# Kernel optimization log

Measured on AMD Instinct MI355X. Metric: run time of the kernel, lower is better.

The kernel has to match this reference:

```python
import jax, jax.numpy as jnp
import numpy as np

N = 100000      # nodes
E = 1600000     # edges (avg degree 16)
D = 64          # in_channels == conv widths == lin width
G = 64          # graphs in batch
OUT = 10        # out_channels


def setup_inputs() -> dict:
    key = jax.random.key(0)
    ks = jax.random.split(key, 20)
    s = 0.1
    inp = {
        "x": jax.random.normal(ks[0], (N, D), jnp.float32),
        "edge_index": jax.random.randint(ks[1], (2, E), 0, N, dtype=jnp.int64),
        "batch": jnp.sort(jax.random.randint(ks[2], (N,), 0, G, dtype=jnp.int64)),
    }
    k = 3
    for i in range(3):  # 3 SAGEConv layers: lin_l (Wl, bl) on aggregated, lin_r (Wr, no bias) on root
        inp[f"c{i}_Wl"] = jax.random.normal(ks[k], (D, D), jnp.float32) * s; k += 1
        inp[f"c{i}_bl"] = jnp.zeros((D,), jnp.float32)
        inp[f"c{i}_Wr"] = jax.random.normal(ks[k], (D, D), jnp.float32) * s; k += 1
    inp["l0_W"] = jax.random.normal(ks[k], (D, D), jnp.float32) * s; k += 1
    inp["l0_b"] = jnp.zeros((D,), jnp.float32)
    inp["out_W"] = jax.random.normal(ks[k], (D, OUT), jnp.float32) * s; k += 1
    inp["out_b"] = jnp.zeros((OUT,), jnp.float32)
    return inp


def reference(x, edge_index, batch,
              c0_Wl, c0_bl, c0_Wr,
              c1_Wl, c1_bl, c1_Wr,
              c2_Wl, c2_bl, c2_Wr,
              l0_W, l0_b, out_W, out_b):
    src, dst = edge_index[0], edge_index[1]
    # in-degree of each target node (mean conv aggregation), computed once
    deg = jax.ops.segment_sum(jnp.ones((E,), x.dtype), dst, num_segments=N)
    inv_deg = (1.0 / jnp.maximum(deg, 1.0))[:, None]

    def sage(h, Wl, bl, Wr):
        # gather source features, mean-aggregate at targets, then lin_l(agg) + lin_r(h)
        agg = jax.ops.segment_sum(h[src], dst, num_segments=N) * inv_deg
        return agg @ Wl + bl + h @ Wr

    h = jax.nn.relu(sage(x, c0_Wl, c0_bl, c0_Wr))
    h = jax.nn.relu(sage(h, c1_Wl, c1_bl, c1_Wr))
    h = jax.nn.relu(sage(h, c2_Wl, c2_bl, c2_Wr))

    # global mean pool over graphs
    cnt = jax.ops.segment_sum(jnp.ones((N,), h.dtype), batch, num_segments=G)
    g = jax.ops.segment_sum(h, batch, num_segments=G) / jnp.maximum(cnt, 1.0)[:, None]

    g = jax.nn.relu(g @ l0_W + l0_b)
    return g @ out_W + out_b  # [G, OUT]
```

## Files before the change

### kernel.cpp

```cpp
#include <hip/hip_runtime.h>
#include <hip/hip_fp16.h>

#define WPB 8
#define PADK 136
#define BSH 8
#define BNODES 256
#define SC_BLOCKS 256
#define HIST_BLOCKS 256
#define HSTRIDE 512

typedef _Float16 half8 __attribute__((ext_vector_type(8)));
typedef _Float16 half4v __attribute__((ext_vector_type(4)));
typedef float floatx4 __attribute__((ext_vector_type(4)));

__global__ __launch_bounds__(256) void gnn_pre(const int* __restrict__ dst,
                                               int* __restrict__ bkt_cnt, int nbkt, int E,
                                               const int* __restrict__ batch,
                                               float* __restrict__ gcnt, int N,
                                               const float4* __restrict__ xin,
                                               ushort4* __restrict__ x16o, int n4,
                                               __half* __restrict__ x16,
                                               __half* __restrict__ hA,
                                               __half* __restrict__ hB,
                                               int* __restrict__ hist_all) {
    int tid = threadIdx.x;
    if (blockIdx.x < HIST_BLOCKS) {
        __shared__ int h[512];
        __shared__ int gb[64];
        for (int i = tid; i < nbkt; i += 256) h[i] = 0;
        if (tid < 64) gb[tid] = 0;
        __syncthreads();
        const int stride = HIST_BLOCKS * 256;
        if ((E & 3) == 0) {
            const int4* dst4 = (const int4*)dst;
            int E4 = E >> 2;
            for (int e = blockIdx.x * 256 + tid; e < E4; e += stride) {
                int4 d = dst4[e];
                atomicAdd(&h[d.x >> BSH], 1);
                atomicAdd(&h[d.y >> BSH], 1);
                atomicAdd(&h[d.z >> BSH], 1);
                atomicAdd(&h[d.w >> BSH], 1);
            }
        } else {
            for (int e = blockIdx.x * 256 + tid; e < E; e += stride)
                atomicAdd(&h[dst[e] >> BSH], 1);
        }
        for (int i = blockIdx.x * 256 + tid; i < N; i += stride)
            atomicAdd(&gb[batch[i]], 1);
        __syncthreads();
        for (int i = tid; i < nbkt; i += 256) {
            int v = h[i];
            hist_all[blockIdx.x * HSTRIDE + i] = v;
            if (v) atomicAdd(&bkt_cnt[i], v);
        }
        if (tid < 64) {
            int v = gb[tid];
            if (v) atomicAdd(&gcnt[tid], (float)v);
        }
        if (blockIdx.x == 0 && tid < 64) {
            x16[(size_t)N * 64 + tid] = __ushort_as_half((unsigned short)0);
            hA[(size_t)N * 64 + tid] = __ushort_as_half((unsigned short)0);
            hB[(size_t)N * 64 + tid] = __ushort_as_half((unsigned short)0);
        }
    } else {
        int i = (blockIdx.x - HIST_BLOCKS) * 256 + tid;
        if (i < n4) {
            float4 f = xin[i];
            ushort4 o;
            o.x = __half_as_ushort(__float2half(f.x));
            o.y = __half_as_ushort(__float2half(f.y));
            o.z = __half_as_ushort(__float2half(f.z));
            o.w = __half_as_ushort(__float2half(f.w));
            x16o[i] = o;
        }
    }
}

__global__ void gnn_bkt_scan(const int* __restrict__ bkt_cnt, int* __restrict__ bkt_base,
                             int* __restrict__ row_ptr, int nbkt, int N) {
    int lane = threadIdx.x;
    int carry = 0;
    for (int base = 0; base < nbkt; base += 64) {
        int idx = base + lane;
        int v = (idx < nbkt) ? bkt_cnt[idx] : 0;
        int x = v;
#pragma unroll
        for (int off = 1; off < 64; off <<= 1) {
            int y = __shfl_up(x, off);
            if (lane >= off) x += y;
        }
        if (idx < nbkt) bkt_base[idx] = carry + (x - v);
        carry += __shfl(x, 63);
    }
    if (lane == 0) {
        bkt_base[nbkt] = carry;
        row_ptr[N] = carry;
    }
}

__global__ __launch_bounds__(256) void gnn_scan2(const int* __restrict__ hist_all,
                                                 const int* __restrict__ bkt_base,
                                                 int* __restrict__ blk_base_all, int nbkt) {
    int b = blockIdx.x;
    int t = threadIdx.x, lane = t & 63, wv = t >> 6;
    __shared__ int wsum[4];
    int v = hist_all[t * HSTRIDE + b];
    int x = v;
#pragma unroll
    for (int off = 1; off < 64; off <<= 1) {
        int y = __shfl_up(x, off);
        if (lane >= off) x += y;
    }
    if (lane == 63) wsum[wv] = x;
    __syncthreads();
    int wexcl = 0;
    for (int w = 0; w < wv; w++) wexcl += wsum[w];
    blk_base_all[t * HSTRIDE + b] = bkt_base[b] + wexcl + (x - v);
}

__global__ __launch_bounds__(256) void gnn_bkt_scatter(const int* __restrict__ src,
                                                       const int* __restrict__ dst,
                                                       const int* __restrict__ blk_base_all,
                                                       unsigned int* __restrict__ pairs,
                                                       int E, int nbkt) {
    __shared__ int cur[512];
    int tid = threadIdx.x;
    for (int i = tid; i < nbkt; i += 256) cur[i] = blk_base_all[blockIdx.x * HSTRIDE + i];
    __syncthreads();
    const int stride = SC_BLOCKS * 256;
    if ((E & 3) == 0) {
        const int4* dst4 = (const int4*)dst;
        const int4* src4 = (const int4*)src;
        int E4 = E >> 2;
        for (int e = blockIdx.x * 256 + tid; e < E4; e += stride) {
            int4 d = dst4[e];
            int4 s = src4[e];
            int p0 = atomicAdd(&cur[d.x >> BSH], 1);
            pairs[p0] = (unsigned int)s.x | ((unsigned int)(d.x & (BNODES - 1)) << 24);
            int p1 = atomicAdd(&cur[d.y >> BSH], 1);
            pairs[p1] = (unsigned int)s.y | ((unsigned int)(d.y & (BNODES - 1)) << 24);
            int p2 = atomicAdd(&cur[d.z >> BSH], 1);
            pairs[p2] = (unsigned int)s.z | ((unsigned int)(d.z & (BNODES - 1)) << 24);
            int p3 = atomicAdd(&cur[d.w >> BSH], 1);
            pairs[p3] = (unsigned int)s.w | ((unsigned int)(d.w & (BNODES - 1)) << 24);
        }
    } else {
        for (int e = blockIdx.x * 256 + tid; e < E; e += stride) {
            int d = dst[e];
            int b = d >> BSH;
            int p = atomicAdd(&cur[b], 1);
            pairs[p] = (unsigned int)src[e] | ((unsigned int)(d & (BNODES - 1)) << 24);
        }
    }
}

__global__ __launch_bounds__(256) void gnn_bkt_csr(const unsigned int* __restrict__ pairs,
                                                   const int* __restrict__ bkt_base,
                                                   int* __restrict__ row_ptr,
                                                   float* __restrict__ inv_deg,
                                                   int* __restrict__ csr_src, int N) {
    __shared__ int hist[BNODES];
    __shared__ int excl[BNODES];
    __shared__ int cur[BNODES];
    int b = blockIdx.x;
    int base = bkt_base[b];
    int cnt = bkt_base[b + 1] - base;
    int nd0 = b << BSH;
    int tid = threadIdx.x;
    hist[tid] = 0;
    __syncthreads();
    {
        int a0 = (4 - (base & 3)) & 3;
        a0 = min(a0, cnt);
        for (int i = tid; i < a0; i += 256) atomicAdd(&hist[pairs[base + i] >> 24], 1);
        int vcnt = (cnt - a0) >> 2;
        const uint4* p4 = (const uint4*)(pairs + base + a0);
        for (int i = tid; i < vcnt; i += 256) {
            uint4 u = p4[i];
            atomicAdd(&hist[u.x >> 24], 1);
            atomicAdd(&hist[u.y >> 24], 1);
            atomicAdd(&hist[u.z >> 24], 1);
            atomicAdd(&hist[u.w >> 24], 1);
        }
        for (int i = a0 + (vcnt << 2) + tid; i < cnt; i += 256)
            atomicAdd(&hist[pairs[base + i] >> 24], 1);
    }
    __syncthreads();
    if (tid < 64) {
        int carry = 0;
#pragma unroll
        for (int c = 0; c < BNODES; c += 64) {
            int v = hist[c + tid];
            int x = v;
#pragma unroll
            for (int off = 1; off < 64; off <<= 1) {
                int y = __shfl_up(x, off);
                if (tid >= off) x += y;
            }
            excl[c + tid] = carry + (x - v);
            carry += __shfl(x, 63);
        }
    }
    __syncthreads();
    {
        int node = nd0 + tid;
        if (node < N) {
            row_ptr[node] = base + excl[tid];
            int d = hist[tid];
            inv_deg[node] = 1.0f / (float)(d > 1 ? d : 1);
        }
        cur[tid] = excl[tid];
    }
    __syncthreads();
    {
        int a0 = (4 - (base & 3)) & 3;
        a0 = min(a0, cnt);
        for (int i = tid; i < a0; i += 256) {
            unsigned int u = pairs[base + i];
            int pos = atomicAdd(&cur[u >> 24], 1);
            csr_src[base + pos] = (int)(u & 0xFFFFFFu);
        }
        int vcnt = (cnt - a0) >> 2;
        const uint4* p4 = (const uint4*)(pairs + base + a0);
        for (int i = tid; i < vcnt; i += 256) {
            uint4 u = p4[i];
            int pos0 = atomicAdd(&cur[u.x >> 24], 1);
            csr_src[base + pos0] = (int)(u.x & 0xFFFFFFu);
            int pos1 = atomicAdd(&cur[u.y >> 24], 1);
            csr_src[base + pos1] = (int)(u.y & 0xFFFFFFu);
            int pos2 = atomicAdd(&cur[u.z >> 24], 1);
            csr_src[base + pos2] = (int)(u.z & 0xFFFFFFu);
            int pos3 = atomicAdd(&cur[u.w >> 24], 1);
            csr_src[base + pos3] = (int)(u.w & 0xFFFFFFu);
        }
        for (int i = a0 + (vcnt << 2) + tid; i < cnt; i += 256) {
            unsigned int u = pairs[base + i];
            int pos = atomicAdd(&cur[u >> 24], 1);
            csr_src[base + pos] = (int)(u & 0xFFFFFFu);
        }
    }
}

#define LOAD4(eReg, c0, vArr)                                  \
    _Pragma("unroll") for (int c_ = 0; c_ < 4; c_++) {         \
        int sj_ = __shfl(eReg, (c0) + c_ * 4 + quad);          \
        vArr[c_] = hin4v[(size_t)sj_ * 16 + m16];              \
    }
#define ACC4(vArr, accum)                                      \
    _Pragma("unroll") for (int c_ = 0; c_ < 4; c_++) {         \
        accum.x += (float)vArr[c_][0];                         \
        accum.y += (float)vArr[c_][1];                         \
        accum.z += (float)vArr[c_][2];                         \
        accum.w += (float)vArr[c_][3];                         \
    }

__global__ __launch_bounds__(512, 4) void gnn_sage(const __half* __restrict__ hin,
                                                   __half* __restrict__ hout,
                                                   const int* __restrict__ row_ptr,
                                                   const int* __restrict__ csr_src,
                                                   const float* __restrict__ inv_deg,
                                                   const float* __restrict__ Wl,
                                                   const float* __restrict__ bl,
                                                   const float* __restrict__ Wr, int n) {
    __shared__ _Float16 w_lds[64 * PADK];
    __shared__ _Float16 in_lds[WPB][16 * PADK];
    int tid = threadIdx.x, lane = tid & 63, wv = tid >> 6;
    for (int i = tid; i < 64 * 64; i += 512) {
        int k = i >> 6, nn = i & 63;
        w_lds[nn * PADK + k] = (_Float16)Wl[i];
        w_lds[nn * PADK + 64 + k] = (_Float16)Wr[i];
    }
    __syncthreads();
    int ngroups = (n + 15) >> 4;
    int g = blockIdx.x * WPB + wv;
    if (g >= ngroups) return;
    int m16 = lane & 15, quad = lane >> 4;
    int hf = lane >> 5, col = lane & 31;
    float bias[4];
#pragma unroll
    for (int nt = 0; nt < 4; nt++) bias[nt] = bl[nt * 16 + m16];
    _Float16* my_in = in_lds[wv];
    const unsigned* hin32 = (const unsigned*)hin;
    const half4v* hin4v = (const half4v*)hin;
    int nd0 = g << 4;
    int nclamp = n - 1 - nd0;
    int idx = nd0 + lane;
    int rr = (lane <= 16) ? row_ptr[min(idx, n)] : 0;
    float ig = (lane < 16) ? inv_deg[min(idx, n - 1)] : 0.0f;

#pragma unroll
    for (int jp = 0; jp < 8; jp++) {
        int j2 = jp << 1;
        int nd = nd0 + min(j2 + hf, nclamp);
        unsigned u = hin32[(size_t)nd * 32 + col];
        ((unsigned*)(my_in + (j2 + hf) * PADK + 64))[col] = u;
    }

    int ef[16];
#pragma unroll
    for (int j = 0; j < 16; j++) {
        int jj = min(j, nclamp);
        int s0 = __shfl(rr, jj), s1 = __shfl(rr, jj + 1);
        int cb = min(64, s1 - s0);
        ef[j] = (lane < cb) ? csr_src[s0 + lane] : n;
    }

#pragma unroll
    for (int jp = 0; jp < 8; jp++) {
        int j2 = jp << 1;
        int jjA = min(j2, nclamp), jjB = min(j2 + 1, nclamp);
        int s0A = __shfl(rr, jjA), s1A = __shfl(rr, jjA + 1);
        int s0B = __shfl(rr, jjB), s1B = __shfl(rr, jjB + 1);
        float idgA = __shfl(ig, jjA), idgB = __shfl(ig, jjB);
        int cbA = min(64, s1A - s0A), cbB = min(64, s1B - s0B);
        floatx4 accA = {0.f, 0.f, 0.f, 0.f};
        floatx4 accB = {0.f, 0.f, 0.f, 0.f};
        {
            half4v vA[4], vB[4];
            LOAD4(ef[j2], 0, vA);
            LOAD4(ef[j2 + 1], 0, vB);
            ACC4(vA, accA);
            ACC4(vB, accB);
        }
        if (cbA > 16) {
            half4v v0[4];
            LOAD4(ef[j2], 16, v0);
            ACC4(v0, accA);
            if (cbA > 32) { half4v v1[4]; LOAD4(ef[j2], 32, v1); ACC4(v1, accA); }
            if (cbA > 48) { half4v v2[4]; LOAD4(ef[j2], 48, v2); ACC4(v2, accA); }
        }
        if (cbB > 16) {
            half4v v0[4];
            LOAD4(ef[j2 + 1], 16, v0);
            ACC4(v0, accB);
            if (cbB > 32) { half4v v1[4]; LOAD4(ef[j2 + 1], 32, v1); ACC4(v1, accB); }
            if (cbB > 48) { half4v v2[4]; LOAD4(ef[j2 + 1], 48, v2); ACC4(v2, accB); }
        }
        for (int base_ = s0A + 64; base_ < s1A; base_ += 64) {
            int cb = min(64, s1A - base_);
            int ei = (lane < cb) ? csr_src[base_ + lane] : n;
            for (int i0 = 0; i0 < cb; i0 += 16) {
                half4v vt[4];
                LOAD4(ei, i0, vt);
                ACC4(vt, accA);
            }
        }
        for (int base_ = s0B + 64; base_ < s1B; base_ += 64) {
            int cb = min(64, s1B - base_);
            int ei = (lane < cb) ? csr_src[base_ + lane] : n;
            for (int i0 = 0; i0 < cb; i0 += 16) {
                half4v vt[4];
                LOAD4(ei, i0, vt);
                ACC4(vt, accB);
            }
        }
        accA.x += __shfl_xor(accA.x, 16); accA.y += __shfl_xor(accA.y, 16);
        accA.z += __shfl_xor(accA.z, 16); accA.w += __shfl_xor(accA.w, 16);
        accA.x += __shfl_xor(accA.x, 32); accA.y += __shfl_xor(accA.y, 32);
        accA.z += __shfl_xor(accA.z, 32); accA.w += __shfl_xor(accA.w, 32);
        accB.x += __shfl_xor(accB.x, 16); accB.y += __shfl_xor(accB.y, 16);
        accB.z += __shfl_xor(accB.z, 16); accB.w += __shfl_xor(accB.w, 16);
        accB.x += __shfl_xor(accB.x, 32); accB.y += __shfl_xor(accB.y, 32);
        accB.z += __shfl_xor(accB.z, 32); accB.w += __shfl_xor(accB.w, 32);
        if (quad == 0) {
            half4v hw;
            hw[0] = (_Float16)(accA.x * idgA);
            hw[1] = (_Float16)(accA.y * idgA);
            hw[2] = (_Float16)(accA.z * idgA);
            hw[3] = (_Float16)(accA.w * idgA);
            *(half4v*)(my_in + j2 * PADK + m16 * 4) = hw;
        } else if (quad == 1) {
            half4v hw;
            hw[0] = (_Float16)(accB.x * idgB);
            hw[1] = (_Float16)(accB.y * idgB);
            hw[2] = (_Float16)(accB.z * idgB);
            hw[3] = (_Float16)(accB.w * idgB);
            *(half4v*)(my_in + (j2 + 1) * PADK + m16 * 4) = hw;
        }
    }
    half8 afrag[4];
    const _Float16* abase = my_in + m16 * PADK + quad * 8;
#pragma unroll
    for (int ks = 0; ks < 4; ks++) afrag[ks] = *(const half8*)(abase + ks * 32);
    floatx4 accv[4];
#pragma unroll
    for (int nt = 0; nt < 4; nt++) {
        accv[nt].x = 0.f; accv[nt].y = 0.f; accv[nt].z = 0.f; accv[nt].w = 0.f;
    }
#pragma unroll
    for (int nt = 0; nt < 4; nt++) {
        const _Float16* bbase = w_lds + (nt * 16 + m16) * PADK + quad * 8;
#pragma unroll
        for (int ks = 0; ks < 4; ks++) {
            half8 bfrag = *(const half8*)(bbase + ks * 32);
            accv[nt] = __builtin_amdgcn_mfma_f32_16x16x32_f16(afrag[ks], bfrag, accv[nt], 0, 0, 0);
        }
    }
#pragma unroll
    for (int nt = 0; nt < 4; nt++) {
#pragma unroll
        for (int r = 0; r < 4; r++) {
            int node = nd0 + quad * 4 + r;
            if (node < n) {
                float v = fmaxf(accv[nt][r] + bias[nt], 0.0f);
                hout[(size_t)node * 64 + nt * 16 + m16] = __float2half(v);
            }
        }
    }
}

__global__ __launch_bounds__(512, 4) void gnn_sage_pool(const __half* __restrict__ hin,
                                                        const int* __restrict__ row_ptr,
                                                        const int* __restrict__ csr_src,
                                                        const float* __restrict__ inv_deg,
                                                        const float* __restrict__ Wl,
                                                        const float* __restrict__ bl,
                                                        const float* __restrict__ Wr,
                                                        const int* __restrict__ batch,
                                                        float* __restrict__ gsum, int n) {
    __shared__ _Float16 w_lds[64 * PADK];
    __shared__ _Float16 in_lds[WPB][16 * PADK];
    int tid = threadIdx.x, lane = tid & 63, wv = tid >> 6;
    for (int i = tid; i < 64 * 64; i += 512) {
        int k = i >> 6, nn = i & 63;
        w_lds[nn * PADK + k] = (_Float16)Wl[i];
        w_lds[nn * PADK + 64 + k] = (_Float16)Wr[i];
    }
    __syncthreads();
    int ngroups = (n + 15) >> 4;
    int g = blockIdx.x * WPB + wv;
    if (g >= ngroups) return;
    int m16 = lane & 15, quad = lane >> 4;
    int hf = lane >> 5, col = lane & 31;
    float bias[4];
#pragma unroll
    for (int nt = 0; nt < 4; nt++) bias[nt] = bl[nt * 16 + m16];
    _Float16* my_in = in_lds[wv];
    const unsigned* hin32 = (const unsigned*)hin;
    const half4v* hin4v = (const half4v*)hin;
    int nd0 = g << 4;
    int nclamp = n - 1 - nd0;
    int idx = nd0 + lane;
    int rr = (lane <= 16) ? row_ptr[min(idx, n)] : 0;
    float ig = (lane < 16) ? inv_deg[min(idx, n - 1)] : 0.0f;

#pragma unroll
    for (int jp = 0; jp < 8; jp++) {
        int j2 = jp << 1;
        int nd = nd0 + min(j2 + hf, nclamp);
        unsigned u = hin32[(size_t)nd * 32 + col];
        ((unsigned*)(my_in + (j2 + hf) * PADK + 64))[col] = u;
    }

    int ef[16];
#pragma unroll
    for (int j = 0; j < 16; j++) {
        int jj = min(j, nclamp);
        int s0 = __shfl(rr, jj), s1 = __shfl(rr, jj + 1);
        int cb = min(64, s1 - s0);
        ef[j] = (lane < cb) ? csr_src[s0 + lane] : n;
    }

#pragma unroll
    for (int jp = 0; jp < 8; jp++) {
        int j2 = jp << 1;
        int jjA = min(j2, nclamp), jjB = min(j2 + 1, nclamp);
        int s0A = __shfl(rr, jjA), s1A = __shfl(rr, jjA + 1);
        int s0B = __shfl(rr, jjB), s1B = __shfl(rr, jjB + 1);
        float idgA = __shfl(ig, jjA), idgB = __shfl(ig, jjB);
        int cbA = min(64, s1A - s0A), cbB = min(64, s1B - s0B);
        floatx4 accA = {0.f, 0.f, 0.f, 0.f};
        floatx4 accB = {0.f, 0.f, 0.f, 0.f};
        {
            half4v vA[4], vB[4];
            LOAD4(ef[j2], 0, vA);
            LOAD4(ef[j2 + 1], 0, vB);
            ACC4(vA, accA);
            ACC4(vB, accB);
        }
        if (cbA > 16) {
            half4v v0[4];
            LOAD4(ef[j2], 16, v0);
            ACC4(v0, accA);
            if (cbA > 32) { half4v v1[4]; LOAD4(ef[j2], 32, v1); ACC4(v1, accA); }
            if (cbA > 48) { half4v v2[4]; LOAD4(ef[j2], 48, v2); ACC4(v2, accA); }
        }
        if (cbB > 16) {
            half4v v0[4];
            LOAD4(ef[j2 + 1], 16, v0);
            ACC4(v0, accB);
            if (cbB > 32) { half4v v1[4]; LOAD4(ef[j2 + 1], 32, v1); ACC4(v1, accB); }
            if (cbB > 48) { half4v v2[4]; LOAD4(ef[j2 + 1], 48, v2); ACC4(v2, accB); }
        }
        for (int base_ = s0A + 64; base_ < s1A; base_ += 64) {
            int cb = min(64, s1A - base_);
            int ei = (lane < cb) ? csr_src[base_ + lane] : n;
            for (int i0 = 0; i0 < cb; i0 += 16) {
                half4v vt[4];
                LOAD4(ei, i0, vt);
                ACC4(vt, accA);
            }
        }
        for (int base_ = s0B + 64; base_ < s1B; base_ += 64) {
            int cb = min(64, s1B - base_);
            int ei = (lane < cb) ? csr_src[base_ + lane] : n;
            for (int i0 = 0; i0 < cb; i0 += 16) {
                half4v vt[4];
                LOAD4(ei, i0, vt);
                ACC4(vt, accB);
            }
        }
        accA.x += __shfl_xor(accA.x, 16); accA.y += __shfl_xor(accA.y, 16);
        accA.z += __shfl_xor(accA.z, 16); accA.w += __shfl_xor(accA.w, 16);
        accA.x += __shfl_xor(accA.x, 32); accA.y += __shfl_xor(accA.y, 32);
        accA.z += __shfl_xor(accA.z, 32); accA.w += __shfl_xor(accA.w, 32);
        accB.x += __shfl_xor(accB.x, 16); accB.y += __shfl_xor(accB.y, 16);
        accB.z += __shfl_xor(accB.z, 16); accB.w += __shfl_xor(accB.w, 16);
        accB.x += __shfl_xor(accB.x, 32); accB.y += __shfl_xor(accB.y, 32);
        accB.z += __shfl_xor(accB.z, 32); accB.w += __shfl_xor(accB.w, 32);
        if (quad == 0) {
            half4v hw;
            hw[0] = (_Float16)(accA.x * idgA);
            hw[1] = (_Float16)(accA.y * idgA);
            hw[2] = (_Float16)(accA.z * idgA);
            hw[3] = (_Float16)(accA.w * idgA);
            *(half4v*)(my_in + j2 * PADK + m16 * 4) = hw;
        } else if (quad == 1) {
            half4v hw;
            hw[0] = (_Float16)(accB.x * idgB);
            hw[1] = (_Float16)(accB.y * idgB);
            hw[2] = (_Float16)(accB.z * idgB);
            hw[3] = (_Float16)(accB.w * idgB);
            *(half4v*)(my_in + (j2 + 1) * PADK + m16 * 4) = hw;
        }
    }
    half8 afrag[4];
    const _Float16* abase = my_in + m16 * PADK + quad * 8;
#pragma unroll
    for (int ks = 0; ks < 4; ks++) afrag[ks] = *(const half8*)(abase + ks * 32);
    floatx4 accv[4];
#pragma unroll
    for (int nt = 0; nt < 4; nt++) {
        accv[nt].x = 0.f; accv[nt].y = 0.f; accv[nt].z = 0.f; accv[nt].w = 0.f;
    }
#pragma unroll
    for (int nt = 0; nt < 4; nt++) {
        const _Float16* bbase = w_lds + (nt * 16 + m16) * PADK + quad * 8;
#pragma unroll
        for (int ks = 0; ks < 4; ks++) {
            half8 bfrag = *(const half8*)(bbase + ks * 32);
            accv[nt] = __builtin_amdgcn_mfma_f32_16x16x32_f16(afrag[ks], bfrag, accv[nt], 0, 0, 0);
        }
    }
    int bFirst = batch[nd0];
    int bLast = batch[min(nd0 + 15, n - 1)];
    if (bFirst == bLast && nd0 + 15 < n) {
#pragma unroll
        for (int nt = 0; nt < 4; nt++) {
            float s = fmaxf(accv[nt][0] + bias[nt], 0.0f) + fmaxf(accv[nt][1] + bias[nt], 0.0f) +
                      fmaxf(accv[nt][2] + bias[nt], 0.0f) + fmaxf(accv[nt][3] + bias[nt], 0.0f);
            s += __shfl_xor(s, 16);
            s += __shfl_xor(s, 32);
            if (quad == 0) atomicAdd(&gsum[bFirst * 64 + nt * 16 + m16], s);
        }
    } else {
#pragma unroll
        for (int nt = 0; nt < 4; nt++) {
#pragma unroll
            for (int r = 0; r < 4; r++) {
                int node = nd0 + quad * 4 + r;
                if (node < n) {
                    int bg = batch[node];
                    float v = fmaxf(accv[nt][r] + bias[nt], 0.0f);
                    atomicAdd(&gsum[bg * 64 + nt * 16 + m16], v);
                }
            }
        }
    }
}

__global__ __launch_bounds__(1024) void gnn_head(const float* __restrict__ gsum,
                                                 const float* __restrict__ gcnt,
                                                 const float* __restrict__ l0W,
                                                 const float* __restrict__ l0b,
                                                 const float* __restrict__ outW,
                                                 const float* __restrict__ outb,
                                                 float* __restrict__ out, int G, int OUT) {
    __shared__ float gm[64 * 64];
    __shared__ float t2[64 * 64];
    int tid = threadIdx.x;
    for (int i = tid; i < G * 64; i += 1024) {
        int r = i >> 6;
        gm[i] = gsum[i] / fmaxf(gcnt[r], 1.0f);
    }
    __syncthreads();
    for (int i = tid; i < G * 64; i += 1024) {
        int r = i >> 6, c = i & 63;
        float s = l0b[c];
#pragma unroll 8
        for (int k = 0; k < 64; k++) s += gm[(r << 6) + k] * l0W[(k << 6) + c];
        t2[i] = fmaxf(s, 0.0f);
    }
    __syncthreads();
    for (int i = tid; i < G * OUT; i += 1024) {
        int r = i / OUT, c = i - r * OUT;
        float s = outb[c];
#pragma unroll 8
        for (int k = 0; k < 64; k++) s += t2[(r << 6) + k] * outW[k * OUT + c];
        out[i] = s;
    }
}

extern "C" void kernel_launch(void* const* d_in, const int* in_sizes, int n_in,
                              void* d_out, int out_size, void* d_ws, size_t ws_size,
                              hipStream_t stream) {
    const float* x = (const float*)d_in[0];
    const int* ei = (const int*)d_in[1];
    const int* batch = (const int*)d_in[2];
    const float* Wl[3] = {(const float*)d_in[3], (const float*)d_in[6], (const float*)d_in[9]};
    const float* bl[3] = {(const float*)d_in[4], (const float*)d_in[7], (const float*)d_in[10]};
    const float* Wr[3] = {(const float*)d_in[5], (const float*)d_in[8], (const float*)d_in[11]};
    const float* l0W = (const float*)d_in[12];
    const float* l0b = (const float*)d_in[13];
    const float* outW = (const float*)d_in[14];
    const float* outb = (const float*)d_in[15];

    int N = in_sizes[2];
    int E = in_sizes[1] / 2;
    int OUT = 10;
    int G = out_size / OUT;
    const int* src = ei;
    const int* dst = ei + E;
    int NBKT = (N + BNODES - 1) >> BSH;

    char* ws = (char*)d_ws;
    size_t off = 0;
    auto alloc = [&](size_t b) -> char* {
        char* p = ws + off;
        off = (off + b + 255) & ~(size_t)255;
        return p;
    };
    int* row_ptr = (int*)alloc((size_t)(N + 1) * 4);
    int* csr_src = (int*)alloc((size_t)E * 4);
    float* inv_deg = (float*)alloc((size_t)N * 4);
    size_t zoff = off;
    int* bkt_cnt = (int*)alloc((size_t)NBKT * 4);
    float* gcnt = (float*)alloc((size_t)G * 4);
    float* gsum = (float*)alloc((size_t)G * 64 * 4);
    size_t zlen = off - zoff;
    int* bkt_base = (int*)alloc((size_t)(NBKT + 1) * 4);
    int* hist_all = (int*)alloc((size_t)HIST_BLOCKS * HSTRIDE * 4);
    int* blk_base_all = (int*)alloc((size_t)HIST_BLOCKS * HSTRIDE * 4);
    unsigned int* pairs = (unsigned int*)alloc((size_t)E * 4);
    __half* x16 = (__half*)alloc((size_t)(N + 1) * 64 * 2);
    __half* hA = (__half*)alloc((size_t)(N + 1) * 64 * 2);
    __half* hB = (__half*)alloc((size_t)(N + 1) * 64 * 2);

    hipMemsetAsync(ws + zoff, 0, zlen, stream);

    int n4 = N * 64 / 4;
    int pre_blocks = HIST_BLOCKS + (n4 + 255) / 256;
    gnn_pre<<<pre_blocks, 256, 0, stream>>>(dst, bkt_cnt, NBKT, E, batch, gcnt, N,
                                            (const float4*)x, (ushort4*)x16, n4,
                                            x16, hA, hB, hist_all);
    gnn_bkt_scan<<<1, 64, 0, stream>>>(bkt_cnt, bkt_base, row_ptr, NBKT, N);
    gnn_scan2<<<NBKT, 256, 0, stream>>>(hist_all, bkt_base, blk_base_all, NBKT);
    gnn_bkt_scatter<<<SC_BLOCKS, 256, 0, stream>>>(src, dst, blk_base_all, pairs, E, NBKT);
    gnn_bkt_csr<<<NBKT, 256, 0, stream>>>(pairs, bkt_base, row_ptr, inv_deg, csr_src, N);

    int ngroups = (N + 15) >> 4;
    int sage_blocks = (ngroups + WPB - 1) / WPB;
    gnn_sage<<<sage_blocks, 512, 0, stream>>>(x16, hA, row_ptr, csr_src, inv_deg,
                                              Wl[0], bl[0], Wr[0], N);
    gnn_sage<<<sage_blocks, 512, 0, stream>>>(hA, hB, row_ptr, csr_src, inv_deg,
                                              Wl[1], bl[1], Wr[1], N);
    gnn_sage_pool<<<sage_blocks, 512, 0, stream>>>(hB, row_ptr, csr_src, inv_deg,
                                                   Wl[2], bl[2], Wr[2], batch, gsum, N);

    gnn_head<<<1, 1024, 0, stream>>>(gsum, gcnt, l0W, l0b, outW, outb, (float*)d_out, G, OUT);
}
```

Before: 293.5 us.

## Fold bucket scan into scan2 and fuse MLP head into pool kernel

Removes two kernel launches. The single-block bucket prefix scan is dropped: each scan2 block now computes its own bucket base by reducing all preceding bucket counts, and the last block also writes the total. The separate one-block head kernel is folded into the final SAGE pooling kernel through a last-block-done atomic counter, and that last block runs the two small dense layers in reused shared memory. In exchange, scan2 blocks do redundant reduction work, and the head runs with 512 threads instead of 1024.

Result: slower. 304.5 us (+3.7%).

```diff
diff --git a/kernel.cpp b/kernel.cpp
--- a/kernel.cpp
+++ b/kernel.cpp
@@ -76,34 +76,21 @@
     }
 }
 
-__global__ void gnn_bkt_scan(const int* __restrict__ bkt_cnt, int* __restrict__ bkt_base,
-                             int* __restrict__ row_ptr, int nbkt, int N) {
-    int lane = threadIdx.x;
-    int carry = 0;
-    for (int base = 0; base < nbkt; base += 64) {
-        int idx = base + lane;
-        int v = (idx < nbkt) ? bkt_cnt[idx] : 0;
-        int x = v;
-#pragma unroll
-        for (int off = 1; off < 64; off <<= 1) {
-            int y = __shfl_up(x, off);
-            if (lane >= off) x += y;
-        }
-        if (idx < nbkt) bkt_base[idx] = carry + (x - v);
-        carry += __shfl(x, 63);
-    }
-    if (lane == 0) {
-        bkt_base[nbkt] = carry;
-        row_ptr[N] = carry;
-    }
-}
-
 __global__ __launch_bounds__(256) void gnn_scan2(const int* __restrict__ hist_all,
-                                                 const int* __restrict__ bkt_base,
-                                                 int* __restrict__ blk_base_all, int nbkt) {
+                                                 const int* __restrict__ bkt_cnt,
+                                                 int* __restrict__ bkt_base,
+                                                 int* __restrict__ row_ptr,
+                                                 int* __restrict__ blk_base_all,
+                                                 int nbkt, int N) {
     int b = blockIdx.x;
     int t = threadIdx.x, lane = t & 63, wv = t >> 6;
     __shared__ int wsum[4];
+    __shared__ int red[4];
+    int part = 0;
+    for (int i = t; i < b; i += 256) part += bkt_cnt[i];
+#pragma unroll
+    for (int off = 1; off < 64; off <<= 1) part += __shfl_xor(part, off);
+    if (lane == 0) red[wv] = part;
     int v = hist_all[t * HSTRIDE + b];
     int x = v;
 #pragma unroll
@@ -113,9 +100,18 @@
     }
     if (lane == 63) wsum[wv] = x;
     __syncthreads();
+    int base = red[0] + red[1] + red[2] + red[3];
     int wexcl = 0;
     for (int w = 0; w < wv; w++) wexcl += wsum[w];
-    blk_base_all[t * HSTRIDE + b] = bkt_base[b] + wexcl + (x - v);
+    blk_base_all[t * HSTRIDE + b] = base + wexcl + (x - v);
+    if (t == 0) {
+        bkt_base[b] = base;
+        if (b == nbkt - 1) {
+            int tot = base + bkt_cnt[b];
+            bkt_base[nbkt] = tot;
+            row_ptr[N] = tot;
+        }
+    }
 }
 
 __global__ __launch_bounds__(256) void gnn_bkt_scatter(const int* __restrict__ src,
@@ -417,9 +413,18 @@
                                                         const float* __restrict__ bl,
                                                         const float* __restrict__ Wr,
                                                         const int* __restrict__ batch,
-                                                        float* __restrict__ gsum, int n) {
+                                                        float* __restrict__ gsum,
+                                                        const float* __restrict__ gcnt,
+                                                        const float* __restrict__ l0W,
+                                                        const float* __restrict__ l0b,
+                                                        const float* __restrict__ outW,
+                                                        const float* __restrict__ outb,
+                                                        float* __restrict__ out,
+                                                        unsigned int* __restrict__ done,
+                                                        int G, int OUT, int n) {
     __shared__ _Float16 w_lds[64 * PADK];
     __shared__ _Float16 in_lds[WPB][16 * PADK];
+    __shared__ int lastsh;
     int tid = threadIdx.x, lane = tid & 63, wv = tid >> 6;
     for (int i = tid; i < 64 * 64; i += 512) {
         int k = i >> 6, nn = i & 63;
@@ -429,185 +434,186 @@
     __syncthreads();
     int ngroups = (n + 15) >> 4;
     int g = blockIdx.x * WPB + wv;
-    if (g >= ngroups) return;
     int m16 = lane & 15, quad = lane >> 4;
     int hf = lane >> 5, col = lane & 31;
-    float bias[4];
-#pragma unroll
-    for (int nt = 0; nt < 4; nt++) bias[nt] = bl[nt * 16 + m16];
-    _Float16* my_in = in_lds[wv];
     const unsigned* hin32 = (const unsigned*)hin;
     const half4v* hin4v = (const half4v*)hin;
-    int nd0 = g << 4;
-    int nclamp = n - 1 - nd0;
-    int idx = nd0 + lane;
-    int rr = (lane <= 16) ? row_ptr[min(idx, n)] : 0;
-    float ig = (lane < 16) ? inv_deg[min(idx, n - 1)] : 0.0f;
-
-#pragma unroll
-    for (int jp = 0; jp < 8; jp++) {
-        int j2 = jp << 1;
-        int nd = nd0 + min(j2 + hf, nclamp);
-        unsigned u = hin32[(size_t)nd * 32 + col];
-        ((unsigned*)(my_in + (j2 + hf) * PADK + 64))[col] = u;
-    }
-
-    int ef[16];
-#pragma unroll
-    for (int j = 0; j < 16; j++) {
-        int jj = min(j, nclamp);
-        int s0 = __shfl(rr, jj), s1 = __shfl(rr, jj + 1);
-        int cb = min(64, s1 - s0);
-        ef[j] = (lane < cb) ? csr_src[s0 + lane] : n;
-    }
-
-#pragma unroll
-    for (int jp = 0; jp < 8; jp++) {
-        int j2 = jp << 1;
-        int jjA = min(j2, nclamp), jjB = min(j2 + 1, nclamp);
-        int s0A = __shfl(rr, jjA), s1A = __shfl(rr, jjA + 1);
-        int s0B = __shfl(rr, jjB), s1B = __shfl(rr, jjB + 1);
-        float idgA = __shfl(ig, jjA), idgB = __shfl(ig, jjB);
-        int cbA = min(64, s1A - s0A), cbB = min(64, s1B - s0B);
-        floatx4 accA = {0.f, 0.f, 0.f, 0.f};
-        floatx4 accB = {0.f, 0.f, 0.f, 0.f};
-        {
-            half4v vA[4], vB[4];
-            LOAD4(ef[j2], 0, vA);
-            LOAD4(ef[j2 + 1], 0, vB);
-            ACC4(vA, accA);
-            ACC4(vB, accB);
-        }
-        if (cbA > 16) {
-            half4v v0[4];
-            LOAD4(ef[j2], 16, v0);
-            ACC4(v0, accA);
-            if (cbA > 32) { half4v v1[4]; LOAD4(ef[j2], 32, v1); ACC4(v1, accA); }
-            if (cbA > 48) { half4v v2[4]; LOAD4(ef[j2], 48, v2); ACC4(v2, accA); }
-        }
-        if (cbB > 16) {
-            half4v v0[4];
-            LOAD4(ef[j2 + 1], 16, v0);
-            ACC4(v0, accB);
-            if (cbB > 32) { half4v v1[4]; LOAD4(ef[j2 + 1], 32, v1); ACC4(v1, accB); }
-            if (cbB > 48) { half4v v2[4]; LOAD4(ef[j2 + 1], 48, v2); ACC4(v2, accB); }
-        }
-        for (int base_ = s0A + 64; base_ < s1A; base_ += 64) {
-            int cb = min(64, s1A - base_);
-            int ei = (lane < cb) ? csr_src[base_ + lane] : n;
-            for (int i0 = 0; i0 < cb; i0 += 16) {
-                half4v vt[4];
-                LOAD4(ei, i0, vt);
-                ACC4(vt, accA);
-            }
-        }
-        for (int base_ = s0B + 64; base_ < s1B; base_ += 64) {
-            int cb = min(64, s1B - base_);
-            int ei = (lane < cb) ? csr_src[base_ + lane] : n;
-            for (int i0 = 0; i0 < cb; i0 += 16) {
-                half4v vt[4];
-                LOAD4(ei, i0, vt);
-                ACC4(vt, accB);
-            }
-        }
-        accA.x += __shfl_xor(accA.x, 16); accA.y += __shfl_xor(accA.y, 16);
-        accA.z += __shfl_xor(accA.z, 16); accA.w += __shfl_xor(accA.w, 16);
-        accA.x += __shfl_xor(accA.x, 32); accA.y += __shfl_xor(accA.y, 32);
-        accA.z += __shfl_xor(accA.z, 32); accA.w += __shfl_xor(accA.w, 32);
-        accB.x += __shfl_xor(accB.x, 16); accB.y += __shfl_xor(accB.y, 16);
-        accB.z += __shfl_xor(accB.z, 16); accB.w += __shfl_xor(accB.w, 16);
-        accB.x += __shfl_xor(accB.x, 32); accB.y += __shfl_xor(accB.y, 32);
-        accB.z += __shfl_xor(accB.z, 32); accB.w += __shfl_xor(accB.w, 32);
-        if (quad == 0) {
-            half4v hw;
-            hw[0] = (_Float16)(accA.x * idgA);
-            hw[1] = (_Float16)(accA.y * idgA);
-            hw[2] = (_Float16)(accA.z * idgA);
-            hw[3] = (_Float16)(accA.w * idgA);
-            *(half4v*)(my_in + j2 * PADK + m16 * 4) = hw;
-        } else if (quad == 1) {
-            half4v hw;
-            hw[0] = (_Float16)(accB.x * idgB);
-            hw[1] = (_Float16)(accB.y * idgB);
-            hw[2] = (_Float16)(accB.z * idgB);
-            hw[3] = (_Float16)(accB.w * idgB);
-            *(half4v*)(my_in + (j2 + 1) * PADK + m16 * 4) = hw;
-        }
-    }
-    half8 afrag[4];
-    const _Float16* abase = my_in + m16 * PADK + quad * 8;
-#pragma unroll
-    for (int ks = 0; ks < 4; ks++) afrag[ks] = *(const half8*)(abase + ks * 32);
-    floatx4 accv[4];
-#pragma unroll
-    for (int nt = 0; nt < 4; nt++) {
-        accv[nt].x = 0.f; accv[nt].y = 0.f; accv[nt].z = 0.f; accv[nt].w = 0.f;
-    }
-#pragma unroll
-    for (int nt = 0; nt < 4; nt++) {
-        const _Float16* bbase = w_lds + (nt * 16 + m16) * PADK + quad * 8;
-#pragma unroll
-        for (int ks = 0; ks < 4; ks++) {
-            half8 bfrag = *(const half8*)(bbase + ks * 32);
-            accv[nt] = __builtin_amdgcn_mfma_f32_16x16x32_f16(afrag[ks], bfrag, accv[nt], 0, 0, 0);
-        }
-    }
-    int bFirst = batch[nd0];
-    int bLast = batch[min(nd0 + 15, n - 1)];
-    if (bFirst == bLast && nd0 + 15 < n) {
+    if (g < ngroups) {
+        float bias[4];
+#pragma unroll
+        for (int nt = 0; nt < 4; nt++) bias[nt] = bl[nt * 16 + m16];
+        _Float16* my_in = in_lds[wv];
+        int nd0 = g << 4;
+        int nclamp = n - 1 - nd0;
+        int idx = nd0 + lane;
+        int rr = (lane <= 16) ? row_ptr[min(idx, n)] : 0;
+        float ig = (lane < 16) ? inv_deg[min(idx, n - 1)] : 0.0f;
+
+#pragma unroll
+        for (int jp = 0; jp < 8; jp++) {
+            int j2 = jp << 1;
+            int nd = nd0 + min(j2 + hf, nclamp);
+            unsigned u = hin32[(size_t)nd * 32 + col];
+            ((unsigned*)(my_in + (j2 + hf) * PADK + 64))[col] = u;
+        }
+
+        int ef[16];
+#pragma unroll
+        for (int j = 0; j < 16; j++) {
+            int jj = min(j, nclamp);
+            int s0 = __shfl(rr, jj), s1 = __shfl(rr, jj + 1);
+            int cb = min(64, s1 - s0);
+            ef[j] = (lane < cb) ? csr_src[s0 + lane] : n;
+        }
+
+#pragma unroll
+        for (int jp = 0; jp < 8; jp++) {
+            int j2 = jp << 1;
+            int jjA = min(j2, nclamp), jjB = min(j2 + 1, nclamp);
+            int s0A = __shfl(rr, jjA), s1A = __shfl(rr, jjA + 1);
+            int s0B = __shfl(rr, jjB), s1B = __shfl(rr, jjB + 1);
+            float idgA = __shfl(ig, jjA), idgB = __shfl(ig, jjB);
+            int cbA = min(64, s1A - s0A), cbB = min(64, s1B - s0B);
+            floatx4 accA = {0.f, 0.f, 0.f, 0.f};
+            floatx4 accB = {0.f, 0.f, 0.f, 0.f};
+            {
+                half4v vA[4], vB[4];
+                LOAD4(ef[j2], 0, vA);
+                LOAD4(ef[j2 + 1], 0, vB);
+                ACC4(vA, accA);
+                ACC4(vB, accB);
+            }
+            if (cbA > 16) {
+                half4v v0[4];
+                LOAD4(ef[j2], 16, v0);
+                ACC4(v0, accA);
+                if (cbA > 32) { half4v v1[4]; LOAD4(ef[j2], 32, v1); ACC4(v1, accA); }
+                if (cbA > 48) { half4v v2[4]; LOAD4(ef[j2], 48, v2); ACC4(v2, accA); }
+            }
+            if (cbB > 16) {
+                half4v v0[4];
+                LOAD4(ef[j2 + 1], 16, v0);
+                ACC4(v0, accB);
+                if (cbB > 32) { half4v v1[4]; LOAD4(ef[j2 + 1], 32, v1); ACC4(v1, accB); }
+                if (cbB > 48) { half4v v2[4]; LOAD4(ef[j2 + 1], 48, v2); ACC4(v2, accB); }
+            }
+            for (int base_ = s0A + 64; base_ < s1A; base_ += 64) {
+                int cb = min(64, s1A - base_);
+                int ei = (lane < cb) ? csr_src[base_ + lane] : n;
+                for (int i0 = 0; i0 < cb; i0 += 16) {
+                    half4v vt[4];
+                    LOAD4(ei, i0, vt);
+                    ACC4(vt, accA);
+                }
+            }
+            for (int base_ = s0B + 64; base_ < s1B; base_ += 64) {
+                int cb = min(64, s1B - base_);
+                int ei = (lane < cb) ? csr_src[base_ + lane] : n;
+                for (int i0 = 0; i0 < cb; i0 += 16) {
+                    half4v vt[4];
+                    LOAD4(ei, i0, vt);
+                    ACC4(vt, accB);
+                }
+            }
+            accA.x += __shfl_xor(accA.x, 16); accA.y += __shfl_xor(accA.y, 16);
+            accA.z += __shfl_xor(accA.z, 16); accA.w += __shfl_xor(accA.w, 16);
+            accA.x += __shfl_xor(accA.x, 32); accA.y += __shfl_xor(accA.y, 32);
+            accA.z += __shfl_xor(accA.z, 32); accA.w += __shfl_xor(accA.w, 32);
+            accB.x += __shfl_xor(accB.x, 16); accB.y += __shfl_xor(accB.y, 16);
+            accB.z += __shfl_xor(accB.z, 16); accB.w += __shfl_xor(accB.w, 16);
+            accB.x += __shfl_xor(accB.x, 32); accB.y += __shfl_xor(accB.y, 32);
+            accB.z += __shfl_xor(accB.z, 32); accB.w += __shfl_xor(accB.w, 32);
+            if (quad == 0) {
+                half4v hw;
+                hw[0] = (_Float16)(accA.x * idgA);
+                hw[1] = (_Float16)(accA.y * idgA);
+                hw[2] = (_Float16)(accA.z * idgA);
+                hw[3] = (_Float16)(accA.w * idgA);
+                *(half4v*)(my_in + j2 * PADK + m16 * 4) = hw;
+            } else if (quad == 1) {
+                half4v hw;
+                hw[0] = (_Float16)(accB.x * idgB);
+                hw[1] = (_Float16)(accB.y * idgB);
+                hw[2] = (_Float16)(accB.z * idgB);
+                hw[3] = (_Float16)(accB.w * idgB);
+                *(half4v*)(my_in + (j2 + 1) * PADK + m16 * 4) = hw;
+            }
+        }
+        half8 afrag[4];
+        const _Float16* abase = my_in + m16 * PADK + quad * 8;
+#pragma unroll
+        for (int ks = 0; ks < 4; ks++) afrag[ks] = *(const half8*)(abase + ks * 32);
+        floatx4 accv[4];
 #pragma unroll
         for (int nt = 0; nt < 4; nt++) {
-            float s = fmaxf(accv[nt][0] + bias[nt], 0.0f) + fmaxf(accv[nt][1] + bias[nt], 0.0f) +
-                      fmaxf(accv[nt][2] + bias[nt], 0.0f) + fmaxf(accv[nt][3] + bias[nt], 0.0f);
-            s += __shfl_xor(s, 16);
-            s += __shfl_xor(s, 32);
-            if (quad == 0) atomicAdd(&gsum[bFirst * 64 + nt * 16 + m16], s);
-        }
-    } else {
+            accv[nt].x = 0.f; accv[nt].y = 0.f; accv[nt].z = 0.f; accv[nt].w = 0.f;
+        }
 #pragma unroll
         for (int nt = 0; nt < 4; nt++) {
-#pragma unroll
-            for (int r = 0; r < 4; r++) {
-                int node = nd0 + quad * 4 + r;
-                if (node < n) {
-                    int bg = batch[node];
-                    float v = fmaxf(accv[nt][r] + bias[nt], 0.0f);
-                    atomicAdd(&gsum[bg * 64 + nt * 16 + m16], v);
+            const _Float16* bbase = w_lds + (nt * 16 + m16) * PADK + quad * 8;
+#pragma unroll
+            for (int ks = 0; ks < 4; ks++) {
+                half8 bfrag = *(const half8*)(bbase + ks * 32);
+                accv[nt] = __builtin_amdgcn_mfma_f32_16x16x32_f16(afrag[ks], bfrag, accv[nt], 0, 0, 0);
+            }
+        }
+        int bFirst = batch[nd0];
+        int bLast = batch[min(nd0 + 15, n - 1)];
+        if (bFirst == bLast && nd0 + 15 < n) {
+#pragma unroll
+            for (int nt = 0; nt < 4; nt++) {
+                float s = fmaxf(accv[nt][0] + bias[nt], 0.0f) + fmaxf(accv[nt][1] + bias[nt], 0.0f) +
+                          fmaxf(accv[nt][2] + bias[nt], 0.0f) + fmaxf(accv[nt][3] + bias[nt], 0.0f);
+                s += __shfl_xor(s, 16);
+                s += __shfl_xor(s, 32);
+                if (quad == 0) atomicAdd(&gsum[bFirst * 64 + nt * 16 + m16], s);
+            }
+        } else {
+#pragma unroll
+            for (int nt = 0; nt < 4; nt++) {
+#pragma unroll
+                for (int r = 0; r < 4; r++) {
+                    int node = nd0 + quad * 4 + r;
+                    if (node < n) {
+                        int bg = batch[node];
+                        float v = fmaxf(accv[nt][r] + bias[nt], 0.0f);
+                        atomicAdd(&gsum[bg * 64 + nt * 16 + m16], v);
+                    }
                 }
             }
         }
     }
-}
-
-__global__ __launch_bounds__(1024) void gnn_head(const float* __restrict__ gsum,
-                                                 const float* __restrict__ gcnt,
-                                                 const float* __restrict__ l0W,
-                                                 const float* __restrict__ l0b,
-                                                 const float* __restrict__ outW,
-                                                 const float* __restrict__ outb,
-                                                 float* __restrict__ out, int G, int OUT) {
-    __shared__ float gm[64 * 64];
-    __shared__ float t2[64 * 64];
-    int tid = threadIdx.x;
-    for (int i = tid; i < G * 64; i += 1024) {
-        int r = i >> 6;
-        gm[i] = gsum[i] / fmaxf(gcnt[r], 1.0f);
-    }
-    __syncthreads();
-    for (int i = tid; i < G * 64; i += 1024) {
-        int r = i >> 6, c = i & 63;
-        float s = l0b[c];
+    __syncthreads();
+    if (tid == 0) {
+        __threadfence();
+        unsigned int old = atomicAdd(done, 1u);
+        lastsh = (old == gridDim.x - 1) ? 1 : 0;
+    }
+    __syncthreads();
+    if (lastsh) {
+        float* gm = (float*)&in_lds[0][0];
+        float* t2 = gm + 64 * 64;
+        for (int i = tid; i < G * 64; i += 512) {
+            int r = i >> 6;
+            float s = atomicAdd(&gsum[i], 0.0f);
+            gm[i] = s / fmaxf(gcnt[r], 1.0f);
+        }
+        __syncthreads();
+        for (int i = tid; i < G * 64; i += 512) {
+            int r = i >> 6, c = i & 63;
+            float s = l0b[c];
 #pragma unroll 8
-        for (int k = 0; k < 64; k++) s += gm[(r << 6) + k] * l0W[(k << 6) + c];
-        t2[i] = fmaxf(s, 0.0f);
-    }
-    __syncthreads();
-    for (int i = tid; i < G * OUT; i += 1024) {
-        int r = i / OUT, c = i - r * OUT;
-        float s = outb[c];
+            for (int k = 0; k < 64; k++) s += gm[(r << 6) + k] * l0W[(k << 6) + c];
+            t2[i] = fmaxf(s, 0.0f);
+        }
+        __syncthreads();
+        for (int i = tid; i < G * OUT; i += 512) {
+            int r = i / OUT, c = i - r * OUT;
+            float s = outb[c];
 #pragma unroll 8
-        for (int k = 0; k < 64; k++) s += t2[(r << 6) + k] * outW[k * OUT + c];
-        out[i] = s;
+            for (int k = 0; k < 64; k++) s += t2[(r << 6) + k] * outW[k * OUT + c];
+            out[i] = s;
+        }
     }
 }
 
@@ -647,6 +653,7 @@
     int* bkt_cnt = (int*)alloc((size_t)NBKT * 4);
     float* gcnt = (float*)alloc((size_t)G * 4);
     float* gsum = (float*)alloc((size_t)G * 64 * 4);
+    unsigned int* done = (unsigned int*)alloc(4);
     size_t zlen = off - zoff;
     int* bkt_base = (int*)alloc((size_t)(NBKT + 1) * 4);
     int* hist_all = (int*)alloc((size_t)HIST_BLOCKS * HSTRIDE * 4);
@@ -663,8 +670,8 @@
     gnn_pre<<<pre_blocks, 256, 0, stream>>>(dst, bkt_cnt, NBKT, E, batch, gcnt, N,
                                             (const float4*)x, (ushort4*)x16, n4,
                                             x16, hA, hB, hist_all);
-    gnn_bkt_scan<<<1, 64, 0, stream>>>(bkt_cnt, bkt_base, row_ptr, NBKT, N);
-    gnn_scan2<<<NBKT, 256, 0, stream>>>(hist_all, bkt_base, blk_base_all, NBKT);
+    gnn_scan2<<<NBKT, 256, 0, stream>>>(hist_all, bkt_cnt, bkt_base, row_ptr,
+                                        blk_base_all, NBKT, N);
     gnn_bkt_scatter<<<SC_BLOCKS, 256, 0, stream>>>(src, dst, blk_base_all, pairs, E, NBKT);
     gnn_bkt_csr<<<NBKT, 256, 0, stream>>>(pairs, bkt_base, row_ptr, inv_deg, csr_src, N);
 
@@ -675,7 +682,7 @@
     gnn_sage<<<sage_blocks, 512, 0, stream>>>(hA, hB, row_ptr, csr_src, inv_deg,
                                               Wl[1], bl[1], Wr[1], N);
     gnn_sage_pool<<<sage_blocks, 512, 0, stream>>>(hB, row_ptr, csr_src, inv_deg,
-                                                   Wl[2], bl[2], Wr[2], batch, gsum, N);
-
-    gnn_head<<<1, 1024, 0, stream>>>(gsum, gcnt, l0W, l0b, outW, outb, (float*)d_out, G, OUT);
+                                                   Wl[2], bl[2], Wr[2], batch, gsum,
+                                                   gcnt, l0W, l0b, outW, outb,
+                                                   (float*)d_out, done, G, OUT, N);
 }
```
